# Kernel tuning notes

Hardware: AMD Instinct MI355X
Metric: run time of the kernel (lower is better)

The kernel has to match this reference:

```python
import jax, jax.numpy as jnp
import numpy as np

TOP_K = 2
NUM_EXPERTS = 64
LOAD_BALANCE_ALPHA = 0.01
Z_LOSS_ALPHA = 1e-4
TEMPERATURE = 1.0  # buffer init, clamped to [0.1, 2.0] -> 1.0 (seq_len < 8192 branch)


def setup_inputs() -> dict:
    key = jax.random.key(0)
    k1, k2 = jax.random.split(key)
    x = jax.random.normal(k1, (4, 4096, 1024), dtype=jnp.float32)
    gate_w = jax.random.normal(k2, (NUM_EXPERTS, 1024), dtype=jnp.float32) * (1.0 / np.sqrt(1024))
    return {"x": x, "gate_w": gate_w}


def reference(x, gate_w):
    B, S, H = x.shape
    x_flat = x.reshape(-1, H)                      # [T, H], T = B*S
    logits = jnp.einsum('th,eh->te', x_flat, gate_w)  # [T, E]
    logits = logits / TEMPERATURE
    scores = jax.nn.softmax(logits, axis=-1)       # [T, E]
    # eval path: dynamic_top_k == top_k, no noise / capacity limitation
    top_scores, top_idx = jax.lax.top_k(scores, TOP_K)   # [T, K]
    top_scores = jax.nn.softmax(top_scores.astype(jnp.float32), axis=-1).astype(x.dtype)
    # load-balance loss: squared deviation of mean expert load from uniform
    expert_load = scores.mean(axis=0)              # [E]
    ideal = 1.0 / NUM_EXPERTS
    lb_loss = LOAD_BALANCE_ALPHA * NUM_EXPERTS * jnp.sum((expert_load - ideal) ** 2)
    # z-loss: mean squared logsumexp of gate logits
    z = jax.nn.logsumexp(logits, axis=-1)          # [T]
    z_loss = Z_LOSS_ALPHA * jnp.mean(z ** 2)
    total_loss = lb_loss + z_loss
    return top_scores, top_idx, total_loss
```

## Files before the change

kernel.cpp:

```cpp
#include <hip/hip_runtime.h>
#include <math.h>

#define T_TOK 16384
#define H_DIM 1024
#define NEXP  64


__global__ void moe_prep(const float* __restrict__ gw, float* __restrict__ ws) {
    int tid = blockIdx.x * blockDim.x + threadIdx.x;
    if (tid < 128) ws[tid] = 0.f;
    int e = tid >> 10;
    int k = tid & 1023;
    ws[128 + k * 64 + e] = gw[tid];
}

__launch_bounds__(512)
__global__ void moe_main(const float* __restrict__ x,
                         const float* __restrict__ wt,
                         float* __restrict__ acc_ws,
                         float* __restrict__ out) {
    __shared__ float xbuf[2][4096];
    __shared__ float sc[64][65];
    __shared__ float row_inv[64];
    __shared__ float colpart[8][64];

    const int tid  = threadIdx.x;
    const int lane = tid & 63;
    const int wv   = tid >> 6;
    const int g = __builtin_amdgcn_readfirstlane(wv & 3);
    const int h = __builtin_amdgcn_readfirstlane(wv >> 2);
    const int tok0 = blockIdx.x << 6;

    const float* gp[4];
    int lds_off[4];
#pragma unroll
    for (int j = 0; j < 4; ++j) {
        int cid  = (wv << 8) + (j << 6) + lane;
        int tile = cid >> 10;
        int rr   = (cid & 1023) >> 4;
        int cg   = cid & 15;
        gp[j] = x + ((size_t)(tok0 + rr) << 10) + (tile << 9) + (cg << 2);
        lds_off[j] = (tile << 12) + (rr << 6) + ((cg ^ (rr & 15)) << 2);
    }

    float acc[16];
#pragma unroll
    for (int e = 0; e < 16; ++e) acc[e] = 0.f;

    float4 pf[4];
#pragma unroll
    for (int j = 0; j < 4; ++j) pf[j] = *(const float4*)gp[j];

    float* xb = &xbuf[0][0];
    const int swz = lane & 15;
    const float* xrow = &xbuf[h][lane << 6];

#pragma unroll 1
    for (int s = 0; s < 8; ++s) {
        __syncthreads();
#pragma unroll
        for (int j = 0; j < 4; ++j) *(float4*)(xb + lds_off[j]) = pf[j];
        __syncthreads();
        if (s < 7) {
#pragma unroll
            for (int j = 0; j < 4; ++j)
                pf[j] = *(const float4*)(gp[j] + ((s + 1) << 6));
        }
        const float* wrow = wt + (((h << 9) + (s << 6)) << 6) + (g << 4);
#pragma unroll
        for (int c = 0; c < 16; ++c) {
            float4 xv = *(const float4*)(xrow + ((c ^ swz) << 2));
            float xa[4] = {xv.x, xv.y, xv.z, xv.w};
#pragma unroll
            for (int j = 0; j < 4; ++j) {
                const float* wkj = wrow + (((c << 2) + j) << 6);
                float xj = xa[j];
#pragma unroll
                for (int e = 0; e < 16; ++e)
                    acc[e] = fmaf(xj, wkj[e], acc[e]);
            }
        }
    }

    if (h == 0) {
#pragma unroll
        for (int e = 0; e < 16; ++e) sc[lane][(g << 4) + e] = acc[e];
    }
    __syncthreads();
    if (h == 1) {
#pragma unroll
        for (int e = 0; e < 16; ++e) sc[lane][(g << 4) + e] += acc[e];
    }
    __syncthreads();

    if (tid < 64) {
        const int r = tid;
        float v1 = -1e30f, v2 = -1e30f;
        int i1 = 0, i2 = 0;
        for (int j = 0; j < 64; ++j) {
            float l = sc[r][j];
            if (l > v1)      { v2 = v1; i2 = i1; v1 = l; i1 = j; }
            else if (l > v2) { v2 = l; i2 = j; }
        }
        float m = v1;
        float ssum = 0.f;
        for (int j = 0; j < 64; ++j) {
            float ev = expf(sc[r][j] - m);
            ssum += ev;
            sc[r][j] = ev;
        }
        float inv = 1.f / ssum;
        row_inv[r] = inv;
        float z = m + logf(ssum);
        float zsq = z * z;
#pragma unroll
        for (int off = 32; off > 0; off >>= 1) zsq += __shfl_down(zsq, off);
        if (lane == 0) atomicAdd(acc_ws + 64, zsq);

        float p1 = inv;
        float p2 = expf(v2 - m) * inv;
        float b  = expf(p2 - p1);
        float s1 = 1.f / (1.f + b);
        float s2 = b * s1;
        int t = tok0 + r;
        out[2 * t]     = s1;
        out[2 * t + 1] = s2;
        out[2 * T_TOK + 2 * t]     = (float)i1;
        out[2 * T_TOK + 2 * t + 1] = (float)i2;
    }
    __syncthreads();

    {
        int e  = tid & 63;
        int rg = tid >> 6;
        float sum = 0.f;
#pragma unroll
        for (int r2 = 0; r2 < 8; ++r2) {
            int row = (rg << 3) + r2;
            sum += sc[row][e] * row_inv[row];
        }
        colpart[rg][e] = sum;
    }
    __syncthreads();
    if (tid < 64) {
        float tot = 0.f;
#pragma unroll
        for (int rg = 0; rg < 8; ++rg) tot += colpart[rg][tid];
        atomicAdd(acc_ws + tid, tot);
    }
}

__global__ void moe_finalize(const float* __restrict__ acc_ws,
                             float* __restrict__ out) {
    int e = threadIdx.x;
    float load = acc_ws[e] * (1.f / 16384.f);
    float d = load - (1.f / 64.f);
    float v = d * d;
#pragma unroll
    for (int off = 32; off > 0; off >>= 1) v += __shfl_down(v, off);
    if (e == 0) {
        float lb = 0.01f * 64.f * v;
        float zl = 1e-4f * acc_ws[64] * (1.f / 16384.f);
        out[4 * T_TOK] = lb + zl;
    }
}

extern "C" void kernel_launch(void* const* d_in, const int* in_sizes, int n_in,
                              void* d_out, int out_size, void* d_ws, size_t ws_size,
                              hipStream_t stream) {
    const float* x  = (const float*)d_in[0];
    const float* gw = (const float*)d_in[1];
    float* out = (float*)d_out;
    float* ws  = (float*)d_ws;

    moe_prep<<<256, 256, 0, stream>>>(gw, ws);
    moe_main<<<256, 512, 0, stream>>>(x, ws + 128, ws, out);
    moe_finalize<<<1, 64, 0, stream>>>(ws, out);
}
```

Before: 156.9 us.

## Double-buffer x tiles in LDS, parallelize top-k/softmax epilogue, tile weight transpose

Result: slower. 255.9 us (+63.1%).

```diff
diff --git a/kernel.cpp b/kernel.cpp
--- a/kernel.cpp
+++ b/kernel.cpp
@@ -2,16 +2,27 @@
 #include <math.h>
 
 #define T_TOK 16384
-#define H_DIM 1024
 #define NEXP  64
 
 
 __global__ void moe_prep(const float* __restrict__ gw, float* __restrict__ ws) {
-    int tid = blockIdx.x * blockDim.x + threadIdx.x;
-    if (tid < 128) ws[tid] = 0.f;
-    int e = tid >> 10;
-    int k = tid & 1023;
-    ws[128 + k * 64 + e] = gw[tid];
+    __shared__ float tile[64][65];
+    const int b = blockIdx.x;
+    const int tid = threadIdx.x;
+    if (b == 0 && tid < 128) ws[tid] = 0.f;
+#pragma unroll
+    for (int it = 0; it < 16; ++it) {
+        int idx = it * 256 + tid;
+        int e = idx >> 6, kk = idx & 63;
+        tile[e][kk] = gw[e * 1024 + b * 64 + kk];
+    }
+    __syncthreads();
+#pragma unroll
+    for (int it = 0; it < 16; ++it) {
+        int idx = it * 256 + tid;
+        int kk = idx >> 6, e = idx & 63;
+        ws[128 + (b * 64 + kk) * 64 + e] = tile[e][kk];
+    }
 }
 
 __launch_bounds__(512)
@@ -19,8 +30,11 @@
                          const float* __restrict__ wt,
                          float* __restrict__ acc_ws,
                          float* __restrict__ out) {
-    __shared__ float xbuf[2][4096];
+    __shared__ float xbuf[2][2][4096];
     __shared__ float sc[64][65];
+    __shared__ float c_v1[8][64], c_i1[8][64], c_v2[8][64], c_i2[8][64];
+    __shared__ float psum[8][64];
+    __shared__ float row_max[64];
     __shared__ float row_inv[64];
     __shared__ float colpart[8][64];
 
@@ -31,54 +45,63 @@
     const int h = __builtin_amdgcn_readfirstlane(wv >> 2);
     const int tok0 = blockIdx.x << 6;
 
-    const float* gp[4];
-    int lds_off[4];
-#pragma unroll
-    for (int j = 0; j < 4; ++j) {
-        int cid  = (wv << 8) + (j << 6) + lane;
-        int tile = cid >> 10;
-        int rr   = (cid & 1023) >> 4;
-        int cg   = cid & 15;
-        gp[j] = x + ((size_t)(tok0 + rr) << 10) + (tile << 9) + (cg << 2);
-        lds_off[j] = (tile << 12) + (rr << 6) + ((cg ^ (rr & 15)) << 2);
-    }
+    const int tile = wv >> 2;
+    const int rr0  = ((wv & 3) << 4) + (lane >> 4);
+    const int cg   = lane & 15;
+    const float* gbase = x + (((size_t)(tok0 + rr0)) << 10) + (tile << 9) + (cg << 2);
+    const int lo0 = (tile << 12) + ((rr0 +  0) << 6) + ((cg ^ ((rr0 +  0) & 15)) << 2);
+    const int lo1 = (tile << 12) + ((rr0 +  4) << 6) + ((cg ^ ((rr0 +  4) & 15)) << 2);
+    const int lo2 = (tile << 12) + ((rr0 +  8) << 6) + ((cg ^ ((rr0 +  8) & 15)) << 2);
+    const int lo3 = (tile << 12) + ((rr0 + 12) << 6) + ((cg ^ ((rr0 + 12) & 15)) << 2);
+    float* xb = &xbuf[0][0][0];
 
     float acc[16];
 #pragma unroll
     for (int e = 0; e < 16; ++e) acc[e] = 0.f;
 
-    float4 pf[4];
-#pragma unroll
-    for (int j = 0; j < 4; ++j) pf[j] = *(const float4*)gp[j];
-
-    float* xb = &xbuf[0][0];
-    const int swz = lane & 15;
-    const float* xrow = &xbuf[h][lane << 6];
+    float4 p0 = *(const float4*)(gbase);
+    float4 p1 = *(const float4*)(gbase + 4096);
+    float4 p2 = *(const float4*)(gbase + 8192);
+    float4 p3 = *(const float4*)(gbase + 12288);
+    *(float4*)(xb + lo0) = p0;
+    *(float4*)(xb + lo1) = p1;
+    *(float4*)(xb + lo2) = p2;
+    *(float4*)(xb + lo3) = p3;
+
+    const int swz = cg;
+    const float* xrow_base = &xbuf[0][h][lane << 6];
 
 #pragma unroll 1
     for (int s = 0; s < 8; ++s) {
         __syncthreads();
-#pragma unroll
-        for (int j = 0; j < 4; ++j) *(float4*)(xb + lds_off[j]) = pf[j];
-        __syncthreads();
         if (s < 7) {
-#pragma unroll
-            for (int j = 0; j < 4; ++j)
-                pf[j] = *(const float4*)(gp[j] + ((s + 1) << 6));
-        }
+            const float* gs = gbase + ((s + 1) << 6);
+            p0 = *(const float4*)(gs);
+            p1 = *(const float4*)(gs + 4096);
+            p2 = *(const float4*)(gs + 8192);
+            p3 = *(const float4*)(gs + 12288);
+        }
+        const float* xrow = xrow_base + ((s & 1) << 13);
         const float* wrow = wt + (((h << 9) + (s << 6)) << 6) + (g << 4);
 #pragma unroll
         for (int c = 0; c < 16; ++c) {
             float4 xv = *(const float4*)(xrow + ((c ^ swz) << 2));
-            float xa[4] = {xv.x, xv.y, xv.z, xv.w};
-#pragma unroll
-            for (int j = 0; j < 4; ++j) {
-                const float* wkj = wrow + (((c << 2) + j) << 6);
-                float xj = xa[j];
-#pragma unroll
-                for (int e = 0; e < 16; ++e)
-                    acc[e] = fmaf(xj, wkj[e], acc[e]);
-            }
+            const float* w0 = wrow + ((c << 2) << 6);
+#pragma unroll
+            for (int e = 0; e < 16; ++e) acc[e] = fmaf(xv.x, w0[e],       acc[e]);
+#pragma unroll
+            for (int e = 0; e < 16; ++e) acc[e] = fmaf(xv.y, w0[64 + e],  acc[e]);
+#pragma unroll
+            for (int e = 0; e < 16; ++e) acc[e] = fmaf(xv.z, w0[128 + e], acc[e]);
+#pragma unroll
+            for (int e = 0; e < 16; ++e) acc[e] = fmaf(xv.w, w0[192 + e], acc[e]);
+        }
+        if (s < 7) {
+            float* xd = xb + ((~s & 1) << 13);
+            *(float4*)(xd + lo0) = p0;
+            *(float4*)(xd + lo1) = p1;
+            *(float4*)(xd + lo2) = p2;
+            *(float4*)(xd + lo3) = p3;
         }
     }
 
@@ -93,40 +116,72 @@
     }
     __syncthreads();
 
+    {
+        int t = tid >> 3, sub = tid & 7;
+        float v1 = -1e30f, v2 = -1e30f; int i1 = 0, i2 = 0;
+#pragma unroll
+        for (int j = 0; j < 8; ++j) {
+            int e = sub * 8 + j;
+            float l = sc[t][e];
+            if (l > v1)      { v2 = v1; i2 = i1; v1 = l; i1 = e; }
+            else if (l > v2) { v2 = l; i2 = e; }
+        }
+        c_v1[sub][t] = v1; c_i1[sub][t] = (float)i1;
+        c_v2[sub][t] = v2; c_i2[sub][t] = (float)i2;
+    }
+    __syncthreads();
+    float tv1 = -1e30f, tv2 = -1e30f; int ti1 = 0, ti2 = 0;
     if (tid < 64) {
-        const int r = tid;
-        float v1 = -1e30f, v2 = -1e30f;
-        int i1 = 0, i2 = 0;
-        for (int j = 0; j < 64; ++j) {
-            float l = sc[r][j];
-            if (l > v1)      { v2 = v1; i2 = i1; v1 = l; i1 = j; }
-            else if (l > v2) { v2 = l; i2 = j; }
-        }
-        float m = v1;
+        int t = tid;
+#pragma unroll
+        for (int sub = 0; sub < 8; ++sub) {
+            float a1 = c_v1[sub][t]; int a1i = (int)c_i1[sub][t];
+            float a2 = c_v2[sub][t]; int a2i = (int)c_i2[sub][t];
+            if (a1 > tv1) {
+                tv2 = tv1; ti2 = ti1; tv1 = a1; ti1 = a1i;
+                if (a2 > tv2) { tv2 = a2; ti2 = a2i; }
+            } else if (a1 > tv2) { tv2 = a1; ti2 = a1i; }
+        }
+        row_max[t] = tv1;
+    }
+    __syncthreads();
+    {
+        int t = tid >> 3, sub = tid & 7;
+        float m = row_max[t];
         float ssum = 0.f;
-        for (int j = 0; j < 64; ++j) {
-            float ev = expf(sc[r][j] - m);
+#pragma unroll
+        for (int j = 0; j < 8; ++j) {
+            int e = sub * 8 + j;
+            float ev = expf(sc[t][e] - m);
+            sc[t][e] = ev;
             ssum += ev;
-            sc[r][j] = ev;
-        }
+        }
+        psum[sub][t] = ssum;
+    }
+    __syncthreads();
+    if (tid < 64) {
+        int t = tid;
+        float ssum = 0.f;
+#pragma unroll
+        for (int sub = 0; sub < 8; ++sub) ssum += psum[sub][t];
         float inv = 1.f / ssum;
-        row_inv[r] = inv;
-        float z = m + logf(ssum);
+        row_inv[t] = inv;
+        float z = row_max[t] + logf(ssum);
         float zsq = z * z;
 #pragma unroll
         for (int off = 32; off > 0; off >>= 1) zsq += __shfl_down(zsq, off);
         if (lane == 0) atomicAdd(acc_ws + 64, zsq);
 
-        float p1 = inv;
-        float p2 = expf(v2 - m) * inv;
-        float b  = expf(p2 - p1);
-        float s1 = 1.f / (1.f + b);
-        float s2 = b * s1;
-        int t = tok0 + r;
-        out[2 * t]     = s1;
-        out[2 * t + 1] = s2;
-        out[2 * T_TOK + 2 * t]     = (float)i1;
-        out[2 * T_TOK + 2 * t + 1] = (float)i2;
+        float p1s = inv;
+        float p2s = expf(tv2 - tv1) * inv;
+        float bb  = expf(p2s - p1s);
+        float s1 = 1.f / (1.f + bb);
+        float s2 = bb * s1;
+        int tk = tok0 + t;
+        out[2 * tk]     = s1;
+        out[2 * tk + 1] = s2;
+        out[2 * T_TOK + 2 * tk]     = (float)ti1;
+        out[2 * T_TOK + 2 * tk + 1] = (float)ti2;
     }
     __syncthreads();
 
@@ -173,7 +228,7 @@
     float* out = (float*)d_out;
     float* ws  = (float*)d_ws;
 
-    moe_prep<<<256, 256, 0, stream>>>(gw, ws);
+    moe_prep<<<16, 256, 0, stream>>>(gw, ws);
     moe_main<<<256, 512, 0, stream>>>(x, ws + 128, ws, out);
     moe_finalize<<<1, 64, 0, stream>>>(ws, out);
 }
```

## Fuse finalize into main kernel via last-block counter, tile transpose in prep

Applied to the files above, without the earlier changes.

Result: faster. 146.0 us (-7.0%).

```diff
diff --git a/kernel.cpp b/kernel.cpp
--- a/kernel.cpp
+++ b/kernel.cpp
@@ -2,19 +2,30 @@
 #include <math.h>
 
 #define T_TOK 16384
-#define H_DIM 1024
 #define NEXP  64
 
 
 __global__ void moe_prep(const float* __restrict__ gw, float* __restrict__ ws) {
-    int tid = blockIdx.x * blockDim.x + threadIdx.x;
-    if (tid < 128) ws[tid] = 0.f;
-    int e = tid >> 10;
-    int k = tid & 1023;
-    ws[128 + k * 64 + e] = gw[tid];
+    __shared__ float tile[64][65];
+    const int b = blockIdx.x;
+    const int tid = threadIdx.x;
+    if (b == 0 && tid < 128) ws[tid] = 0.f;
+#pragma unroll
+    for (int it = 0; it < 16; ++it) {
+        int idx = it * 256 + tid;
+        int e = idx >> 6, kk = idx & 63;
+        tile[e][kk] = gw[e * 1024 + b * 64 + kk];
+    }
+    __syncthreads();
+#pragma unroll
+    for (int it = 0; it < 16; ++it) {
+        int idx = it * 256 + tid;
+        int kk = idx >> 6, e = idx & 63;
+        ws[128 + (b * 64 + kk) * 64 + e] = tile[e][kk];
+    }
 }
 
-__launch_bounds__(512)
+__launch_bounds__(512, 2)
 __global__ void moe_main(const float* __restrict__ x,
                          const float* __restrict__ wt,
                          float* __restrict__ acc_ws,
@@ -23,6 +34,7 @@
     __shared__ float sc[64][65];
     __shared__ float row_inv[64];
     __shared__ float colpart[8][64];
+    __shared__ int   is_last;
 
     const int tid  = threadIdx.x;
     const int lane = tid & 63;
@@ -31,40 +43,42 @@
     const int h = __builtin_amdgcn_readfirstlane(wv >> 2);
     const int tok0 = blockIdx.x << 6;
 
-    const float* gp[4];
-    int lds_off[4];
-#pragma unroll
-    for (int j = 0; j < 4; ++j) {
-        int cid  = (wv << 8) + (j << 6) + lane;
-        int tile = cid >> 10;
-        int rr   = (cid & 1023) >> 4;
-        int cg   = cid & 15;
-        gp[j] = x + ((size_t)(tok0 + rr) << 10) + (tile << 9) + (cg << 2);
-        lds_off[j] = (tile << 12) + (rr << 6) + ((cg ^ (rr & 15)) << 2);
-    }
+    const int tile = wv >> 2;
+    const int rr0  = ((wv & 3) << 4) + (lane >> 4);
+    const int cg   = lane & 15;
+    const float* gbase = x + (((size_t)(tok0 + rr0)) << 10) + (tile << 9) + (cg << 2);
+    const int lo0 = (tile << 12) + ((rr0 +  0) << 6) + ((cg ^ ((rr0 +  0) & 15)) << 2);
+    const int lo1 = (tile << 12) + ((rr0 +  4) << 6) + ((cg ^ ((rr0 +  4) & 15)) << 2);
+    const int lo2 = (tile << 12) + ((rr0 +  8) << 6) + ((cg ^ ((rr0 +  8) & 15)) << 2);
+    const int lo3 = (tile << 12) + ((rr0 + 12) << 6) + ((cg ^ ((rr0 + 12) & 15)) << 2);
+    float* xb = &xbuf[0][0];
 
     float acc[16];
 #pragma unroll
     for (int e = 0; e < 16; ++e) acc[e] = 0.f;
 
-    float4 pf[4];
-#pragma unroll
-    for (int j = 0; j < 4; ++j) pf[j] = *(const float4*)gp[j];
-
-    float* xb = &xbuf[0][0];
-    const int swz = lane & 15;
+    float4 p0 = *(const float4*)(gbase);
+    float4 p1 = *(const float4*)(gbase + 4096);
+    float4 p2 = *(const float4*)(gbase + 8192);
+    float4 p3 = *(const float4*)(gbase + 12288);
+
+    const int swz = cg;
     const float* xrow = &xbuf[h][lane << 6];
 
 #pragma unroll 1
     for (int s = 0; s < 8; ++s) {
         __syncthreads();
-#pragma unroll
-        for (int j = 0; j < 4; ++j) *(float4*)(xb + lds_off[j]) = pf[j];
+        *(float4*)(xb + lo0) = p0;
+        *(float4*)(xb + lo1) = p1;
+        *(float4*)(xb + lo2) = p2;
+        *(float4*)(xb + lo3) = p3;
         __syncthreads();
         if (s < 7) {
-#pragma unroll
-            for (int j = 0; j < 4; ++j)
-                pf[j] = *(const float4*)(gp[j] + ((s + 1) << 6));
+            const float* gs = gbase + ((s + 1) << 6);
+            p0 = *(const float4*)(gs);
+            p1 = *(const float4*)(gs + 4096);
+            p2 = *(const float4*)(gs + 8192);
+            p3 = *(const float4*)(gs + 12288);
         }
         const float* wrow = wt + (((h << 9) + (s << 6)) << 6) + (g << 4);
 #pragma unroll
@@ -117,11 +131,11 @@
         for (int off = 32; off > 0; off >>= 1) zsq += __shfl_down(zsq, off);
         if (lane == 0) atomicAdd(acc_ws + 64, zsq);
 
-        float p1 = inv;
-        float p2 = expf(v2 - m) * inv;
-        float b  = expf(p2 - p1);
-        float s1 = 1.f / (1.f + b);
-        float s2 = b * s1;
+        float p1s = inv;
+        float p2s = expf(v2 - m) * inv;
+        float bb  = expf(p2s - p1s);
+        float s1 = 1.f / (1.f + bb);
+        float s2 = bb * s1;
         int t = tok0 + r;
         out[2 * t]     = s1;
         out[2 * t + 1] = s2;
@@ -148,20 +162,30 @@
         for (int rg = 0; rg < 8; ++rg) tot += colpart[rg][tid];
         atomicAdd(acc_ws + tid, tot);
     }
-}
-
-__global__ void moe_finalize(const float* __restrict__ acc_ws,
-                             float* __restrict__ out) {
-    int e = threadIdx.x;
-    float load = acc_ws[e] * (1.f / 16384.f);
-    float d = load - (1.f / 64.f);
-    float v = d * d;
-#pragma unroll
-    for (int off = 32; off > 0; off >>= 1) v += __shfl_down(v, off);
-    if (e == 0) {
-        float lb = 0.01f * 64.f * v;
-        float zl = 1e-4f * acc_ws[64] * (1.f / 16384.f);
-        out[4 * T_TOK] = lb + zl;
+
+    __syncthreads();
+    if (tid == 0) {
+        __threadfence();
+        int old = __hip_atomic_fetch_add((int*)(acc_ws + 66), 1,
+                                         __ATOMIC_ACQ_REL, __HIP_MEMORY_SCOPE_AGENT);
+        is_last = (old == 255) ? 1 : 0;
+    }
+    __syncthreads();
+    if (is_last && tid < 64) {
+        __threadfence();
+        float load = __hip_atomic_load(acc_ws + tid, __ATOMIC_RELAXED,
+                                       __HIP_MEMORY_SCOPE_AGENT) * (1.f / 16384.f);
+        float d = load - (1.f / 64.f);
+        float v = d * d;
+#pragma unroll
+        for (int off = 32; off > 0; off >>= 1) v += __shfl_down(v, off);
+        if (tid == 0) {
+            float zsum = __hip_atomic_load(acc_ws + 64, __ATOMIC_RELAXED,
+                                           __HIP_MEMORY_SCOPE_AGENT);
+            float lb = 0.01f * 64.f * v;
+            float zl = 1e-4f * zsum * (1.f / 16384.f);
+            out[4 * T_TOK] = lb + zl;
+        }
     }
 }
 
@@ -173,7 +197,6 @@
     float* out = (float*)d_out;
     float* ws  = (float*)d_ws;
 
-    moe_prep<<<256, 256, 0, stream>>>(gw, ws);
+    moe_prep<<<16, 256, 0, stream>>>(gw, ws);
     moe_main<<<256, 512, 0, stream>>>(x, ws + 128, ws, out);
-    moe_finalize<<<1, 64, 0, stream>>>(ws, out);
 }
```
